# Kernel tuning notes

Measured on AMD Instinct MI355X. Metric: run time of the kernel, lower is better.

## Reference

```python
import jax, jax.numpy as jnp
import numpy as np

B, T, I, H, L, O = 4096, 1000, 3, 10, 3, 1


def setup_inputs() -> dict:
    key = jax.random.key(0)
    ks = jax.random.split(key, 1 + 4 * L + 2)
    x = jax.random.normal(ks[0], (B, T, I), dtype=jnp.float32)
    k = 1.0 / np.sqrt(H)
    inp = {"x": x}
    for l in range(L):
        in_dim = I if l == 0 else H
        inp[f"Wih{l}"] = jax.random.uniform(ks[1 + 4 * l], (3 * H, in_dim), minval=-k, maxval=k, dtype=jnp.float32)
        inp[f"Whh{l}"] = jax.random.uniform(ks[2 + 4 * l], (3 * H, H), minval=-k, maxval=k, dtype=jnp.float32)
        inp[f"bih{l}"] = jax.random.uniform(ks[3 + 4 * l], (3 * H,), minval=-k, maxval=k, dtype=jnp.float32)
        inp[f"bhh{l}"] = jax.random.uniform(ks[4 + 4 * l], (3 * H,), minval=-k, maxval=k, dtype=jnp.float32)
    inp["Wout"] = jax.random.uniform(ks[-2], (O, H), minval=-k, maxval=k, dtype=jnp.float32)
    inp["bout"] = jax.random.uniform(ks[-1], (O,), minval=-k, maxval=k, dtype=jnp.float32)
    return inp


def _gru_layer(x, Wih, Whh, bih, bhh):
    # x: [B, T, in]. Precompute input-side gates with one big GEMM.
    xg = jnp.einsum('bti,gi->btg', x, Wih) + bih  # [B, T, 3H]
    h0 = jnp.zeros((x.shape[0], H), dtype=x.dtype)

    def step(h, xt):
        hg = h @ Whh.T + bhh                       # [B, 3H]
        xr, xz, xn = jnp.split(xt, 3, axis=-1)
        hr, hz, hn = jnp.split(hg, 3, axis=-1)
        r = jax.nn.sigmoid(xr + hr)
        z = jax.nn.sigmoid(xz + hz)
        n = jnp.tanh(xn + r * hn)
        h_new = (1.0 - z) * n + z * h
        return h_new, h_new

    _, hs = jax.lax.scan(step, h0, xg.transpose(1, 0, 2))  # [T, B, H]
    return hs.transpose(1, 0, 2)                            # [B, T, H]


def reference(x, Wih0, Whh0, bih0, bhh0, Wih1, Whh1, bih1, bhh1, Wih2, Whh2, bih2, bhh2, Wout, bout):
    h = _gru_layer(x, Wih0, Whh0, bih0, bhh0)
    h = _gru_layer(h, Wih1, Whh1, bih1, bhh1)
    h = _gru_layer(h, Wih2, Whh2, bih2, bhh2)
    last = h[:, -1, :]                      # [B, H]
    return last @ Wout.T + bout             # [B, O]
```

## Files before the change

kernel.cpp:

```cpp
#include <hip/hip_runtime.h>
#include <cstdint>

#define B_SZ 4096
#define T_SZ 1000
#define I_SZ 3
#define H_SZ 10
#define GPW  6
#define STRIDE 36

__device__ __forceinline__ float fsig(float s) {
    float e = __expf(-s);
    return __builtin_amdgcn_rcpf(1.0f + e);
}
__device__ __forceinline__ float ftanh(float y) {
    float e2 = __expf(y + y);
    return 1.0f - 2.0f * __builtin_amdgcn_rcpf(e2 + 1.0f);
}

#define U10(dst, q0, q1, q2) \
    const float dst##0=(q0).x, dst##1=(q0).y, dst##2=(q0).z, dst##3=(q0).w, \
                dst##4=(q1).x, dst##5=(q1).y, dst##6=(q1).z, dst##7=(q1).w, \
                dst##8=(q2).x, dst##9=(q2).y;

#define K15(k) \
    r0  = fmaf(wh0[0][k], a##k, r0);  z0  = fmaf(wh0[1][k], a##k, z0);  nh0 = fmaf(wh0[2][k], a##k, nh0); \
    ri1 = fmaf(wi1[0][k], a##k, ri1); zi1 = fmaf(wi1[1][k], a##k, zi1); nx1 = fmaf(wi1[2][k], a##k, nx1); \
    rh1 = fmaf(wh1[0][k], b##k, rh1); zh1 = fmaf(wh1[1][k], b##k, zh1); nh1 = fmaf(wh1[2][k], b##k, nh1); \
    ri2 = fmaf(wi2[0][k], b##k, ri2); zi2 = fmaf(wi2[1][k], b##k, zi2); nx2 = fmaf(wi2[2][k], b##k, nx2); \
    rh2 = fmaf(wh2[0][k], c##k, rh2); zh2 = fmaf(wh2[1][k], c##k, zh2); nh2 = fmaf(wh2[2][k], c##k, nh2);

__global__ __launch_bounds__(64, 1) void gru3_ilp(
    const float* __restrict__ x,
    const float* __restrict__ Wih0, const float* __restrict__ Whh0,
    const float* __restrict__ bih0, const float* __restrict__ bhh0,
    const float* __restrict__ Wih1, const float* __restrict__ Whh1,
    const float* __restrict__ bih1, const float* __restrict__ bhh1,
    const float* __restrict__ Wih2, const float* __restrict__ Whh2,
    const float* __restrict__ bih2, const float* __restrict__ bhh2,
    const float* __restrict__ Wout, const float* __restrict__ bout,
    float* __restrict__ out)
{
    __shared__ __align__(16) float lds[7 * STRIDE];

    const int lane  = threadIdx.x;
    const int j     = lane % H_SZ;
    const int g     = lane / H_SZ;
    const int b_raw = blockIdx.x * GPW + g;
    const int b     = b_raw < B_SZ ? b_raw : (B_SZ - 1);

    float wi0[3][I_SZ], wh0[3][H_SZ];
    float wi1[3][H_SZ], wh1[3][H_SZ];
    float wi2[3][H_SZ], wh2[3][H_SZ];
#pragma unroll
    for (int gg = 0; gg < 3; ++gg) {
        const int row = gg * H_SZ + j;
#pragma unroll
        for (int i = 0; i < I_SZ; ++i) wi0[gg][i] = Wih0[row * I_SZ + i];
#pragma unroll
        for (int k = 0; k < H_SZ; ++k) wh0[gg][k] = Whh0[row * H_SZ + k];
#pragma unroll
        for (int k = 0; k < H_SZ; ++k) wi1[gg][k] = Wih1[row * H_SZ + k];
#pragma unroll
        for (int k = 0; k < H_SZ; ++k) wh1[gg][k] = Whh1[row * H_SZ + k];
#pragma unroll
        for (int k = 0; k < H_SZ; ++k) wi2[gg][k] = Wih2[row * H_SZ + k];
#pragma unroll
        for (int k = 0; k < H_SZ; ++k) wh2[gg][k] = Whh2[row * H_SZ + k];
    }
#pragma unroll
    for (int gg = 0; gg < 3; ++gg) {
#pragma unroll
        for (int i = 0; i < I_SZ; ++i) asm volatile("" : "+v"(wi0[gg][i]));
#pragma unroll
        for (int k = 0; k < H_SZ; ++k) {
            asm volatile("" : "+v"(wh0[gg][k]));
            asm volatile("" : "+v"(wi1[gg][k]));
            asm volatile("" : "+v"(wh1[gg][k]));
            asm volatile("" : "+v"(wi2[gg][k]));
            asm volatile("" : "+v"(wh2[gg][k]));
        }
    }

    const float br0 = bih0[j] + bhh0[j], bz0 = bih0[H_SZ + j] + bhh0[H_SZ + j];
    const float bni0 = bih0[2 * H_SZ + j], bnh0 = bhh0[2 * H_SZ + j];
    const float br1 = bih1[j] + bhh1[j], bz1 = bih1[H_SZ + j] + bhh1[H_SZ + j];
    const float bni1 = bih1[2 * H_SZ + j], bnh1 = bhh1[2 * H_SZ + j];
    const float br2 = bih2[j] + bhh2[j], bz2 = bih2[H_SZ + j] + bhh2[H_SZ + j];
    const float bni2 = bih2[2 * H_SZ + j], bnh2 = bhh2[2 * H_SZ + j];

    const int gb = g * STRIDE;
    lds[gb + j]      = 0.0f;
    lds[gb + 12 + j] = 0.0f;
    lds[gb + 24 + j] = 0.0f;
    float y0 = 0.0f, y1 = 0.0f, y2 = 0.0f;

    const float* xp = x + (size_t)b * (T_SZ * I_SZ);
    float cx0 = xp[0], cx1 = xp[1], cx2 = xp[2];

    const float4* pa = reinterpret_cast<const float4*>(&lds[gb]);
    const float4* pb = reinterpret_cast<const float4*>(&lds[gb + 12]);
    const float4* pc = reinterpret_cast<const float4*>(&lds[gb + 24]);

    float4 Aq0 = pa[0], Aq1 = pa[1], Aq2 = pa[2];
    float4 Bq0 = pb[0], Bq1 = pb[1], Bq2 = pb[2];
    float4 Cq0 = pc[0], Cq1 = pc[1], Cq2 = pc[2];

#pragma unroll 1
    for (int it = 0; it < T_SZ + 2; ++it) {
        U10(a, Aq0, Aq1, Aq2)
        U10(b, Bq0, Bq1, Bq2)
        U10(c, Cq0, Cq1, Cq2)

        const float x0 = cx0, x1 = cx1, x2 = cx2;
        const int tn = (it + 1 < T_SZ) ? it + 1 : (T_SZ - 1);
        cx0 = xp[tn * 3 + 0];
        cx1 = xp[tn * 3 + 1];
        cx2 = xp[tn * 3 + 2];

        float r0 = br0, z0 = bz0, nx0 = bni0, nh0 = bnh0;
        float ri1 = br1, rh1 = 0.f, zi1 = bz1, zh1 = 0.f, nx1 = bni1, nh1 = bnh1;
        float ri2 = br2, rh2 = 0.f, zi2 = bz2, zh2 = 0.f, nx2 = bni2, nh2 = bnh2;

        r0  = fmaf(wi0[0][0], x0, r0);  r0  = fmaf(wi0[0][1], x1, r0);  r0  = fmaf(wi0[0][2], x2, r0);
        z0  = fmaf(wi0[1][0], x0, z0);  z0  = fmaf(wi0[1][1], x1, z0);  z0  = fmaf(wi0[1][2], x2, z0);
        nx0 = fmaf(wi0[2][0], x0, nx0); nx0 = fmaf(wi0[2][1], x1, nx0); nx0 = fmaf(wi0[2][2], x2, nx0);

        K15(0) K15(1) K15(2) K15(3) K15(4)
        K15(5) K15(6) K15(7) K15(8) K15(9)

        const float ar1 = ri1 + rh1, az1 = zi1 + zh1;
        const float ar2 = ri2 + rh2, az2 = zi2 + zh2;

        const float R0 = fsig(r0),  Z0 = fsig(z0);
        const float R1 = fsig(ar1), Z1 = fsig(az1);
        const float R2 = fsig(ar2), Z2 = fsig(az2);
        const float N0 = ftanh(fmaf(R0, nh0, nx0));
        const float N1 = ftanh(fmaf(R1, nh1, nx1));
        const float N2 = ftanh(fmaf(R2, nh2, nx2));

        const float y0n = fmaf(Z0, y0 - N0, N0);
        const float y1n = fmaf(Z1, y1 - N1, N1);
        const float y2n = fmaf(Z2, y2 - N2, N2);

        y0 = (it < T_SZ)                 ? y0n : y0;
        y1 = (it >= 1 && it <= T_SZ)     ? y1n : y1;
        y2 = (it >= 2)                   ? y2n : y2;

        lds[gb + j]      = y0;
        lds[gb + 12 + j] = y1;
        lds[gb + 24 + j] = y2;

        Aq0 = pa[0]; Aq1 = pa[1]; Aq2 = pa[2];
        Bq0 = pb[0]; Bq1 = pb[1]; Bq2 = pb[2];
        Cq0 = pc[0]; Cq1 = pc[1]; Cq2 = pc[2];
    }

    if (j == 0 && g < GPW && b_raw < B_SZ) {
        const float* hv = &lds[gb + 24];
        float acc = bout[0];
#pragma unroll
        for (int k = 0; k < H_SZ; ++k) acc = fmaf(hv[k], Wout[k], acc);
        out[b_raw] = acc;
    }
}

extern "C" void kernel_launch(void* const* d_in, const int* in_sizes, int n_in,
                              void* d_out, int out_size, void* d_ws, size_t ws_size,
                              hipStream_t stream) {
    const float* x    = (const float*)d_in[0];
    const float* Wih0 = (const float*)d_in[1];
    const float* Whh0 = (const float*)d_in[2];
    const float* bih0 = (const float*)d_in[3];
    const float* bhh0 = (const float*)d_in[4];
    const float* Wih1 = (const float*)d_in[5];
    const float* Whh1 = (const float*)d_in[6];
    const float* bih1 = (const float*)d_in[7];
    const float* bhh1 = (const float*)d_in[8];
    const float* Wih2 = (const float*)d_in[9];
    const float* Whh2 = (const float*)d_in[10];
    const float* bih2 = (const float*)d_in[11];
    const float* bhh2 = (const float*)d_in[12];
    const float* Wout = (const float*)d_in[13];
    const float* bout = (const float*)d_in[14];
    float* out = (float*)d_out;

    const int grid = (B_SZ + GPW - 1) / GPW;
    gru3_ilp<<<grid, 64, 0, stream>>>(x, Wih0, Whh0, bih0, bhh0,
                                      Wih1, Whh1, bih1, bhh1,
                                      Wih2, Whh2, bih2, bhh2,
                                      Wout, bout, out);
}
```

Measured before the change: 601.1 us.

## Split GRU gates across lanes, one gate row per lane with shuffles

Measured after the change: 703.4 us. 1.17x slower.

```diff
diff --git a/kernel.cpp b/kernel.cpp
--- a/kernel.cpp
+++ b/kernel.cpp
@@ -5,8 +5,6 @@
 #define T_SZ 1000
 #define I_SZ 3
 #define H_SZ 10
-#define GPW  6
-#define STRIDE 36
 
 __device__ __forceinline__ float fsig(float s) {
     float e = __expf(-s);
@@ -22,14 +20,14 @@
                 dst##4=(q1).x, dst##5=(q1).y, dst##6=(q1).z, dst##7=(q1).w, \
                 dst##8=(q2).x, dst##9=(q2).y;
 
-#define K15(k) \
-    r0  = fmaf(wh0[0][k], a##k, r0);  z0  = fmaf(wh0[1][k], a##k, z0);  nh0 = fmaf(wh0[2][k], a##k, nh0); \
-    ri1 = fmaf(wi1[0][k], a##k, ri1); zi1 = fmaf(wi1[1][k], a##k, zi1); nx1 = fmaf(wi1[2][k], a##k, nx1); \
-    rh1 = fmaf(wh1[0][k], b##k, rh1); zh1 = fmaf(wh1[1][k], b##k, zh1); nh1 = fmaf(wh1[2][k], b##k, nh1); \
-    ri2 = fmaf(wi2[0][k], b##k, ri2); zi2 = fmaf(wi2[1][k], b##k, zi2); nx2 = fmaf(wi2[2][k], b##k, nx2); \
-    rh2 = fmaf(wh2[0][k], c##k, rh2); zh2 = fmaf(wh2[1][k], c##k, zh2); nh2 = fmaf(wh2[2][k], c##k, nh2);
+#define K5(k) \
+    h0a = fmaf(wh0[k], a##k, h0a); \
+    i1a = fmaf(wi1[k], a##k, i1a); \
+    h1a = fmaf(wh1[k], b##k, h1a); \
+    i2a = fmaf(wi2[k], b##k, i2a); \
+    h2a = fmaf(wh2[k], c##k, h2a);
 
-__global__ __launch_bounds__(64, 1) void gru3_ilp(
+__global__ __launch_bounds__(64, 2) void gru3_rows(
     const float* __restrict__ x,
     const float* __restrict__ Wih0, const float* __restrict__ Whh0,
     const float* __restrict__ bih0, const float* __restrict__ bhh0,
@@ -40,63 +38,45 @@
     const float* __restrict__ Wout, const float* __restrict__ bout,
     float* __restrict__ out)
 {
-    __shared__ __align__(16) float lds[7 * STRIDE];
+    __shared__ __align__(16) float lds[3 * 3 * 12];
 
-    const int lane  = threadIdx.x;
-    const int j     = lane % H_SZ;
-    const int g     = lane / H_SZ;
-    const int b_raw = blockIdx.x * GPW + g;
+    const int lane = threadIdx.x;
+    const int grp  = lane / 30;
+    const int lig  = lane % 30;
+    const int gate = lig / 10;
+    const int u    = lig % 10;
+    const int row  = gate * H_SZ + u;
+    const int b_raw = blockIdx.x * 2 + grp;
     const int b     = b_raw < B_SZ ? b_raw : (B_SZ - 1);
 
-    float wi0[3][I_SZ], wh0[3][H_SZ];
-    float wi1[3][H_SZ], wh1[3][H_SZ];
-    float wi2[3][H_SZ], wh2[3][H_SZ];
+    const int src_r = (lig >= 20) ? (lane - 20) : lane;
+    const int src_z = (lig >= 20) ? (lane - 10) : lane;
+
+    float wi0[I_SZ], wh0[H_SZ];
+    float wi1[H_SZ], wh1[H_SZ];
+    float wi2[H_SZ], wh2[H_SZ];
 #pragma unroll
-    for (int gg = 0; gg < 3; ++gg) {
-        const int row = gg * H_SZ + j;
+    for (int i = 0; i < I_SZ; ++i) wi0[i] = Wih0[row * I_SZ + i];
 #pragma unroll
-        for (int i = 0; i < I_SZ; ++i) wi0[gg][i] = Wih0[row * I_SZ + i];
-#pragma unroll
-        for (int k = 0; k < H_SZ; ++k) wh0[gg][k] = Whh0[row * H_SZ + k];
-#pragma unroll
-        for (int k = 0; k < H_SZ; ++k) wi1[gg][k] = Wih1[row * H_SZ + k];
-#pragma unroll
-        for (int k = 0; k < H_SZ; ++k) wh1[gg][k] = Whh1[row * H_SZ + k];
-#pragma unroll
-        for (int k = 0; k < H_SZ; ++k) wi2[gg][k] = Wih2[row * H_SZ + k];
-#pragma unroll
-        for (int k = 0; k < H_SZ; ++k) wh2[gg][k] = Whh2[row * H_SZ + k];
+    for (int k = 0; k < H_SZ; ++k) {
+        wh0[k] = Whh0[row * H_SZ + k];
+        wi1[k] = Wih1[row * H_SZ + k];
+        wh1[k] = Whh1[row * H_SZ + k];
+        wi2[k] = Wih2[row * H_SZ + k];
+        wh2[k] = Whh2[row * H_SZ + k];
     }
-#pragma unroll
-    for (int gg = 0; gg < 3; ++gg) {
-#pragma unroll
-        for (int i = 0; i < I_SZ; ++i) asm volatile("" : "+v"(wi0[gg][i]));
-#pragma unroll
-        for (int k = 0; k < H_SZ; ++k) {
-            asm volatile("" : "+v"(wh0[gg][k]));
-            asm volatile("" : "+v"(wi1[gg][k]));
-            asm volatile("" : "+v"(wh1[gg][k]));
-            asm volatile("" : "+v"(wi2[gg][k]));
-            asm volatile("" : "+v"(wh2[gg][k]));
-        }
-    }
+    const float bi0 = bih0[row], bh0 = bhh0[row];
+    const float bi1 = bih1[row], bh1 = bhh1[row];
+    const float bi2 = bih2[row], bh2 = bhh2[row];
 
-    const float br0 = bih0[j] + bhh0[j], bz0 = bih0[H_SZ + j] + bhh0[H_SZ + j];
-    const float bni0 = bih0[2 * H_SZ + j], bnh0 = bhh0[2 * H_SZ + j];
-    const float br1 = bih1[j] + bhh1[j], bz1 = bih1[H_SZ + j] + bhh1[H_SZ + j];
-    const float bni1 = bih1[2 * H_SZ + j], bnh1 = bhh1[2 * H_SZ + j];
-    const float br2 = bih2[j] + bhh2[j], bz2 = bih2[H_SZ + j] + bhh2[H_SZ + j];
-    const float bni2 = bih2[2 * H_SZ + j], bnh2 = bhh2[2 * H_SZ + j];
+    for (int i = lane; i < 3 * 3 * 12; i += 64) lds[i] = 0.0f;
 
-    const int gb = g * STRIDE;
-    lds[gb + j]      = 0.0f;
-    lds[gb + 12 + j] = 0.0f;
-    lds[gb + 24 + j] = 0.0f;
-    float y0 = 0.0f, y1 = 0.0f, y2 = 0.0f;
+    float hh0 = 0.0f, hh1 = 0.0f, hh2 = 0.0f;
 
     const float* xp = x + (size_t)b * (T_SZ * I_SZ);
     float cx0 = xp[0], cx1 = xp[1], cx2 = xp[2];
 
+    const int gb = grp * 36;
     const float4* pa = reinterpret_cast<const float4*>(&lds[gb]);
     const float4* pb = reinterpret_cast<const float4*>(&lds[gb + 12]);
     const float4* pc = reinterpret_cast<const float4*>(&lds[gb + 24]);
@@ -117,45 +97,46 @@
         cx1 = xp[tn * 3 + 1];
         cx2 = xp[tn * 3 + 2];
 
-        float r0 = br0, z0 = bz0, nx0 = bni0, nh0 = bnh0;
-        float ri1 = br1, rh1 = 0.f, zi1 = bz1, zh1 = 0.f, nx1 = bni1, nh1 = bnh1;
-        float ri2 = br2, rh2 = 0.f, zi2 = bz2, zh2 = 0.f, nx2 = bni2, nh2 = bnh2;
+        float i0a = bi0, h0a = bh0;
+        float i1a = bi1, h1a = bh1;
+        float i2a = bi2, h2a = bh2;
+        i0a = fmaf(wi0[0], x0, i0a);
+        i0a = fmaf(wi0[1], x1, i0a);
+        i0a = fmaf(wi0[2], x2, i0a);
+        K5(0) K5(1) K5(2) K5(3) K5(4)
+        K5(5) K5(6) K5(7) K5(8) K5(9)
 
-        r0  = fmaf(wi0[0][0], x0, r0);  r0  = fmaf(wi0[0][1], x1, r0);  r0  = fmaf(wi0[0][2], x2, r0);
-        z0  = fmaf(wi0[1][0], x0, z0);  z0  = fmaf(wi0[1][1], x1, z0);  z0  = fmaf(wi0[1][2], x2, z0);
-        nx0 = fmaf(wi0[2][0], x0, nx0); nx0 = fmaf(wi0[2][1], x1, nx0); nx0 = fmaf(wi0[2][2], x2, nx0);
+        const float s0 = fsig(i0a + h0a);
+        const float s1 = fsig(i1a + h1a);
+        const float s2 = fsig(i2a + h2a);
 
-        K15(0) K15(1) K15(2) K15(3) K15(4)
-        K15(5) K15(6) K15(7) K15(8) K15(9)
+        const float r0 = __shfl(s0, src_r), z0 = __shfl(s0, src_z);
+        const float r1 = __shfl(s1, src_r), z1 = __shfl(s1, src_z);
+        const float r2 = __shfl(s2, src_r), z2 = __shfl(s2, src_z);
 
-        const float ar1 = ri1 + rh1, az1 = zi1 + zh1;
-        const float ar2 = ri2 + rh2, az2 = zi2 + zh2;
+        const float n0 = ftanh(fmaf(r0, h0a, i0a));
+        const float n1 = ftanh(fmaf(r1, h1a, i1a));
+        const float n2 = ftanh(fmaf(r2, h2a, i2a));
 
-        const float R0 = fsig(r0),  Z0 = fsig(z0);
-        const float R1 = fsig(ar1), Z1 = fsig(az1);
-        const float R2 = fsig(ar2), Z2 = fsig(az2);
-        const float N0 = ftanh(fmaf(R0, nh0, nx0));
-        const float N1 = ftanh(fmaf(R1, nh1, nx1));
-        const float N2 = ftanh(fmaf(R2, nh2, nx2));
+        const float t0 = fmaf(z0, hh0 - n0, n0);
+        const float t1 = fmaf(z1, hh1 - n1, n1);
+        const float t2 = fmaf(z2, hh2 - n2, n2);
+        hh0 = (it < T_SZ)             ? t0 : hh0;
+        hh1 = (it >= 1 && it <= T_SZ) ? t1 : hh1;
+        hh2 = (it >= 2)               ? t2 : hh2;
 
-        const float y0n = fmaf(Z0, y0 - N0, N0);
-        const float y1n = fmaf(Z1, y1 - N1, N1);
-        const float y2n = fmaf(Z2, y2 - N2, N2);
-
-        y0 = (it < T_SZ)                 ? y0n : y0;
-        y1 = (it >= 1 && it <= T_SZ)     ? y1n : y1;
-        y2 = (it >= 2)                   ? y2n : y2;
-
-        lds[gb + j]      = y0;
-        lds[gb + 12 + j] = y1;
-        lds[gb + 24 + j] = y2;
+        if (lig >= 20) {
+            lds[gb + u]      = hh0;
+            lds[gb + 12 + u] = hh1;
+            lds[gb + 24 + u] = hh2;
+        }
 
         Aq0 = pa[0]; Aq1 = pa[1]; Aq2 = pa[2];
         Bq0 = pb[0]; Bq1 = pb[1]; Bq2 = pb[2];
         Cq0 = pc[0]; Cq1 = pc[1]; Cq2 = pc[2];
     }
 
-    if (j == 0 && g < GPW && b_raw < B_SZ) {
+    if (lig == 0 && grp < 2) {
         const float* hv = &lds[gb + 24];
         float acc = bout[0];
 #pragma unroll
@@ -184,9 +165,9 @@
     const float* bout = (const float*)d_in[14];
     float* out = (float*)d_out;
 
-    const int grid = (B_SZ + GPW - 1) / GPW;
-    gru3_ilp<<<grid, 64, 0, stream>>>(x, Wih0, Whh0, bih0, bhh0,
-                                      Wih1, Whh1, bih1, bhh1,
-                                      Wih2, Whh2, bih2, bhh2,
-                                      Wout, bout, out);
+    const int grid = B_SZ / 2;
+    gru3_rows<<<grid, 64, 0, stream>>>(x, Wih0, Whh0, bih0, bhh0,
+                                       Wih1, Whh1, bih1, bhh1,
+                                       Wih2, Whh2, bih2, bhh2,
+                                       Wout, bout, out);
 }
```

## Move GRU weights from registers into LDS, read as float4 per step

Applied to the files above, without the earlier changes.

After: 1.052 ms. 1.75x slower.

```diff
diff --git a/kernel.cpp b/kernel.cpp
--- a/kernel.cpp
+++ b/kernel.cpp
@@ -6,7 +6,9 @@
 #define I_SZ 3
 #define H_SZ 10
 #define GPW  6
-#define STRIDE 36
+
+#define NW_WORDS (16 * 120)
+#define SH_WORDS (3 * 84)
 
 __device__ __forceinline__ float fsig(float s) {
     float e = __expf(-s);
@@ -17,19 +19,25 @@
     return 1.0f - 2.0f * __builtin_amdgcn_rcpf(e2 + 1.0f);
 }
 
-#define U10(dst, q0, q1, q2) \
-    const float dst##0=(q0).x, dst##1=(q0).y, dst##2=(q0).z, dst##3=(q0).w, \
-                dst##4=(q1).x, dst##5=(q1).y, dst##6=(q1).z, dst##7=(q1).w, \
-                dst##8=(q2).x, dst##9=(q2).y;
+#define LDW(m, g, c) (*(const float4*)(wp + (((m)*3 + (g))*480 + (c)*16)))
+#define FMA4(Q, H, acc) \
+    acc = fmaf((Q).x, (H).x, acc); acc = fmaf((Q).y, (H).y, acc); \
+    acc = fmaf((Q).z, (H).z, acc); acc = fmaf((Q).w, (H).w, acc);
 
-#define K15(k) \
-    r0  = fmaf(wh0[0][k], a##k, r0);  z0  = fmaf(wh0[1][k], a##k, z0);  nh0 = fmaf(wh0[2][k], a##k, nh0); \
-    ri1 = fmaf(wi1[0][k], a##k, ri1); zi1 = fmaf(wi1[1][k], a##k, zi1); nx1 = fmaf(wi1[2][k], a##k, nx1); \
-    rh1 = fmaf(wh1[0][k], b##k, rh1); zh1 = fmaf(wh1[1][k], b##k, zh1); nh1 = fmaf(wh1[2][k], b##k, nh1); \
-    ri2 = fmaf(wi2[0][k], b##k, ri2); zi2 = fmaf(wi2[1][k], b##k, zi2); nx2 = fmaf(wi2[2][k], b##k, nx2); \
-    rh2 = fmaf(wh2[0][k], c##k, rh2); zh2 = fmaf(wh2[1][k], c##k, zh2); nh2 = fmaf(wh2[2][k], c##k, nh2);
+#define WCHUNK(c, HA, HB, HC) do { \
+    const float4 Q00=LDW(0,0,c), Q01=LDW(0,1,c), Q02=LDW(0,2,c); \
+    const float4 Q10=LDW(1,0,c), Q11=LDW(1,1,c), Q12=LDW(1,2,c); \
+    const float4 Q20=LDW(2,0,c), Q21=LDW(2,1,c), Q22=LDW(2,2,c); \
+    const float4 Q30=LDW(3,0,c), Q31=LDW(3,1,c), Q32=LDW(3,2,c); \
+    const float4 Q40=LDW(4,0,c), Q41=LDW(4,1,c), Q42=LDW(4,2,c); \
+    FMA4(Q00, HA, r0)  FMA4(Q01, HA, z0)  FMA4(Q02, HA, nh0) \
+    FMA4(Q10, HA, ri1) FMA4(Q11, HA, zi1) FMA4(Q12, HA, nx1) \
+    FMA4(Q20, HB, rh1) FMA4(Q21, HB, zh1) FMA4(Q22, HB, nh1) \
+    FMA4(Q30, HB, ri2) FMA4(Q31, HB, zi2) FMA4(Q32, HB, nx2) \
+    FMA4(Q40, HC, rh2) FMA4(Q41, HC, zh2) FMA4(Q42, HC, nh2) \
+} while (0)
 
-__global__ __launch_bounds__(64, 1) void gru3_ilp(
+__global__ __launch_bounds__(64, 1) void gru3_ldsw(
     const float* __restrict__ x,
     const float* __restrict__ Wih0, const float* __restrict__ Whh0,
     const float* __restrict__ bih0, const float* __restrict__ bhh0,
@@ -40,7 +48,8 @@
     const float* __restrict__ Wout, const float* __restrict__ bout,
     float* __restrict__ out)
 {
-    __shared__ __align__(16) float lds[7 * STRIDE];
+    __shared__ __align__(16) float sw[NW_WORDS];
+    __shared__ __align__(16) float sh[SH_WORDS];
 
     const int lane  = threadIdx.x;
     const int j     = lane % H_SZ;
@@ -48,68 +57,42 @@
     const int b_raw = blockIdx.x * GPW + g;
     const int b     = b_raw < B_SZ ? b_raw : (B_SZ - 1);
 
-    float wi0[3][I_SZ], wh0[3][H_SZ];
-    float wi1[3][H_SZ], wh1[3][H_SZ];
-    float wi2[3][H_SZ], wh2[3][H_SZ];
-#pragma unroll
-    for (int gg = 0; gg < 3; ++gg) {
-        const int row = gg * H_SZ + j;
-#pragma unroll
-        for (int i = 0; i < I_SZ; ++i) wi0[gg][i] = Wih0[row * I_SZ + i];
-#pragma unroll
-        for (int k = 0; k < H_SZ; ++k) wh0[gg][k] = Whh0[row * H_SZ + k];
-#pragma unroll
-        for (int k = 0; k < H_SZ; ++k) wi1[gg][k] = Wih1[row * H_SZ + k];
-#pragma unroll
-        for (int k = 0; k < H_SZ; ++k) wh1[gg][k] = Whh1[row * H_SZ + k];
-#pragma unroll
-        for (int k = 0; k < H_SZ; ++k) wi2[gg][k] = Wih2[row * H_SZ + k];
-#pragma unroll
-        for (int k = 0; k < H_SZ; ++k) wh2[gg][k] = Whh2[row * H_SZ + k];
-    }
-#pragma unroll
-    for (int gg = 0; gg < 3; ++gg) {
-#pragma unroll
-        for (int i = 0; i < I_SZ; ++i) asm volatile("" : "+v"(wi0[gg][i]));
-#pragma unroll
-        for (int k = 0; k < H_SZ; ++k) {
-            asm volatile("" : "+v"(wh0[gg][k]));
-            asm volatile("" : "+v"(wi1[gg][k]));
-            asm volatile("" : "+v"(wh1[gg][k]));
-            asm volatile("" : "+v"(wi2[gg][k]));
-            asm volatile("" : "+v"(wh2[gg][k]));
-        }
-    }
+    for (int t = lane; t < 300; t += 64) { int r=t/10,k=t%10,gg=r/10,u=r%10; sw[(0*3+gg)*120 + u*12 + k] = Whh0[t]; }
+    for (int t = lane; t < 300; t += 64) { int r=t/10,k=t%10,gg=r/10,u=r%10; sw[(1*3+gg)*120 + u*12 + k] = Wih1[t]; }
+    for (int t = lane; t < 300; t += 64) { int r=t/10,k=t%10,gg=r/10,u=r%10; sw[(2*3+gg)*120 + u*12 + k] = Whh1[t]; }
+    for (int t = lane; t < 300; t += 64) { int r=t/10,k=t%10,gg=r/10,u=r%10; sw[(3*3+gg)*120 + u*12 + k] = Wih2[t]; }
+    for (int t = lane; t < 300; t += 64) { int r=t/10,k=t%10,gg=r/10,u=r%10; sw[(4*3+gg)*120 + u*12 + k] = Whh2[t]; }
+    for (int t = lane; t < 90;  t += 64) { int r=t/3, i=t%3, gg=r/10,u=r%10; sw[15*120 + u*12 + gg*4 + i] = Wih0[t]; }
+    for (int t = lane; t < 150; t += 64) { int tab=t/10,u=t%10; sw[tab*120 + u*12 + 10] = 0.f; sw[tab*120 + u*12 + 11] = 0.f; }
+    for (int t = lane; t < 30;  t += 64) { int u=t/3, c=t%3; sw[15*120 + u*12 + c*4 + 3] = 0.f; }
+    for (int t = lane; t < SH_WORDS; t += 64) sh[t] = 0.0f;
+    __syncthreads();
 
-    const float br0 = bih0[j] + bhh0[j], bz0 = bih0[H_SZ + j] + bhh0[H_SZ + j];
-    const float bni0 = bih0[2 * H_SZ + j], bnh0 = bhh0[2 * H_SZ + j];
-    const float br1 = bih1[j] + bhh1[j], bz1 = bih1[H_SZ + j] + bhh1[H_SZ + j];
-    const float bni1 = bih1[2 * H_SZ + j], bnh1 = bhh1[2 * H_SZ + j];
-    const float br2 = bih2[j] + bhh2[j], bz2 = bih2[H_SZ + j] + bhh2[H_SZ + j];
-    const float bni2 = bih2[2 * H_SZ + j], bnh2 = bhh2[2 * H_SZ + j];
+    const float br0 = bih0[j] + bhh0[j], bz0 = bih0[10 + j] + bhh0[10 + j];
+    const float bni0 = bih0[20 + j], bnh0 = bhh0[20 + j];
+    const float br1 = bih1[j] + bhh1[j], bz1 = bih1[10 + j] + bhh1[10 + j];
+    const float bni1 = bih1[20 + j], bnh1 = bhh1[20 + j];
+    const float br2 = bih2[j] + bhh2[j], bz2 = bih2[10 + j] + bhh2[10 + j];
+    const float bni2 = bih2[20 + j], bnh2 = bhh2[20 + j];
 
-    const int gb = g * STRIDE;
-    lds[gb + j]      = 0.0f;
-    lds[gb + 12 + j] = 0.0f;
-    lds[gb + 24 + j] = 0.0f;
     float y0 = 0.0f, y1 = 0.0f, y2 = 0.0f;
 
     const float* xp = x + (size_t)b * (T_SZ * I_SZ);
     float cx0 = xp[0], cx1 = xp[1], cx2 = xp[2];
 
-    const float4* pa = reinterpret_cast<const float4*>(&lds[gb]);
-    const float4* pb = reinterpret_cast<const float4*>(&lds[gb + 12]);
-    const float4* pc = reinterpret_cast<const float4*>(&lds[gb + 24]);
-
+    const float4* pa = reinterpret_cast<const float4*>(&sh[g * 12]);
+    const float4* pb = reinterpret_cast<const float4*>(&sh[84 + g * 12]);
+    const float4* pc = reinterpret_cast<const float4*>(&sh[168 + g * 12]);
     float4 Aq0 = pa[0], Aq1 = pa[1], Aq2 = pa[2];
     float4 Bq0 = pb[0], Bq1 = pb[1], Bq2 = pb[2];
     float4 Cq0 = pc[0], Cq1 = pc[1], Cq2 = pc[2];
 
+    int aw = j * 48;
+
 #pragma unroll 1
     for (int it = 0; it < T_SZ + 2; ++it) {
-        U10(a, Aq0, Aq1, Aq2)
-        U10(b, Bq0, Bq1, Bq2)
-        U10(c, Cq0, Cq1, Cq2)
+        asm volatile("" : "+v"(aw));
+        const char* wp = (const char*)sw + aw;
 
         const float x0 = cx0, x1 = cx1, x2 = cx2;
         const int tn = (it + 1 < T_SZ) ? it + 1 : (T_SZ - 1);
@@ -121,34 +104,36 @@
         float ri1 = br1, rh1 = 0.f, zi1 = bz1, zh1 = 0.f, nx1 = bni1, nh1 = bnh1;
         float ri2 = br2, rh2 = 0.f, zi2 = bz2, zh2 = 0.f, nx2 = bni2, nh2 = bnh2;
 
-        r0  = fmaf(wi0[0][0], x0, r0);  r0  = fmaf(wi0[0][1], x1, r0);  r0  = fmaf(wi0[0][2], x2, r0);
-        z0  = fmaf(wi0[1][0], x0, z0);  z0  = fmaf(wi0[1][1], x1, z0);  z0  = fmaf(wi0[1][2], x2, z0);
-        nx0 = fmaf(wi0[2][0], x0, nx0); nx0 = fmaf(wi0[2][1], x1, nx0); nx0 = fmaf(wi0[2][2], x2, nx0);
+        {
+            const float4 P0 = *(const float4*)(wp + 15 * 480);
+            const float4 P1 = *(const float4*)(wp + 15 * 480 + 16);
+            const float4 P2 = *(const float4*)(wp + 15 * 480 + 32);
+            r0  = fmaf(P0.x, x0, r0);  r0  = fmaf(P0.y, x1, r0);  r0  = fmaf(P0.z, x2, r0);
+            z0  = fmaf(P1.x, x0, z0);  z0  = fmaf(P1.y, x1, z0);  z0  = fmaf(P1.z, x2, z0);
+            nx0 = fmaf(P2.x, x0, nx0); nx0 = fmaf(P2.y, x1, nx0); nx0 = fmaf(P2.z, x2, nx0);
+        }
 
-        K15(0) K15(1) K15(2) K15(3) K15(4)
-        K15(5) K15(6) K15(7) K15(8) K15(9)
+        WCHUNK(0, Aq0, Bq0, Cq0);
+        WCHUNK(1, Aq1, Bq1, Cq1);
+        WCHUNK(2, Aq2, Bq2, Cq2);
 
-        const float ar1 = ri1 + rh1, az1 = zi1 + zh1;
-        const float ar2 = ri2 + rh2, az2 = zi2 + zh2;
-
-        const float R0 = fsig(r0),  Z0 = fsig(z0);
-        const float R1 = fsig(ar1), Z1 = fsig(az1);
-        const float R2 = fsig(ar2), Z2 = fsig(az2);
+        const float R0 = fsig(r0),        Z0 = fsig(z0);
+        const float R1 = fsig(ri1 + rh1), Z1 = fsig(zi1 + zh1);
+        const float R2 = fsig(ri2 + rh2), Z2 = fsig(zi2 + zh2);
         const float N0 = ftanh(fmaf(R0, nh0, nx0));
         const float N1 = ftanh(fmaf(R1, nh1, nx1));
         const float N2 = ftanh(fmaf(R2, nh2, nx2));
 
-        const float y0n = fmaf(Z0, y0 - N0, N0);
-        const float y1n = fmaf(Z1, y1 - N1, N1);
-        const float y2n = fmaf(Z2, y2 - N2, N2);
+        const float t0 = fmaf(Z0, y0 - N0, N0);
+        const float t1 = fmaf(Z1, y1 - N1, N1);
+        const float t2 = fmaf(Z2, y2 - N2, N2);
+        y0 = (it < T_SZ)             ? t0 : y0;
+        y1 = (it >= 1 && it <= T_SZ) ? t1 : y1;
+        y2 = (it >= 2)               ? t2 : y2;
 
-        y0 = (it < T_SZ)                 ? y0n : y0;
-        y1 = (it >= 1 && it <= T_SZ)     ? y1n : y1;
-        y2 = (it >= 2)                   ? y2n : y2;
-
-        lds[gb + j]      = y0;
-        lds[gb + 12 + j] = y1;
-        lds[gb + 24 + j] = y2;
+        sh[g * 12 + j]       = y0;
+        sh[84 + g * 12 + j]  = y1;
+        sh[168 + g * 12 + j] = y2;
 
         Aq0 = pa[0]; Aq1 = pa[1]; Aq2 = pa[2];
         Bq0 = pb[0]; Bq1 = pb[1]; Bq2 = pb[2];
@@ -156,7 +141,7 @@
     }
 
     if (j == 0 && g < GPW && b_raw < B_SZ) {
-        const float* hv = &lds[gb + 24];
+        const float* hv = &sh[168 + g * 12];
         float acc = bout[0];
 #pragma unroll
         for (int k = 0; k < H_SZ; ++k) acc = fmaf(hv[k], Wout[k], acc);
@@ -185,8 +170,8 @@
     float* out = (float*)d_out;
 
     const int grid = (B_SZ + GPW - 1) / GPW;
-    gru3_ilp<<<grid, 64, 0, stream>>>(x, Wih0, Whh0, bih0, bhh0,
-                                      Wih1, Whh1, bih1, bhh1,
-                                      Wih2, Whh2, bih2, bhh2,
-                                      Wout, bout, out);
+    gru3_ldsw<<<grid, 64, 0, stream>>>(x, Wih0, Whh0, bih0, bhh0,
+                                       Wih1, Whh1, bih1, bhh1,
+                                       Wih2, Whh2, bih2, bhh2,
+                                       Wout, bout, out);
 }
```
